# Kernel tuning notes

Hardware: AMD Instinct MI355X
Metric: run time of the kernel (lower is better)

Reference implementation:

```python
import math
import jax, jax.numpy as jnp
import numpy as np

I_DIM = 64
N_MODES = 16
FACTOR = 4
EPS = 1e-5


def group_norm(x, w, b):
    # x: [B, M, N, C] channels-last; torch GroupNorm(C//16, C) over (group_channels, M, N)
    B, M, N, C = x.shape
    g = C // 16
    xr = x.reshape(B, M, N, g, C // g)
    mean = xr.mean(axis=(1, 2, 4), keepdims=True)
    var = xr.var(axis=(1, 2, 4), keepdims=True)
    xr = (xr - mean) * jax.lax.rsqrt(var + EPS)
    return xr.reshape(B, M, N, C) * w + b


def feed_forward(x, res, l1w, l1b, l2w, l2b, g1w, g1b, g2w, g2b, g3w, g3b):
    h = x @ l1w + l1b                      # [B,M,N,C*factor]
    h = group_norm(h, g1w, g1b)            # fork_1
    h = jax.nn.relu(h)
    h = h @ l2w + l2b                      # [B,M,N,C]
    h = group_norm(h, g2w, g2b)            # fork_2
    h = res + h
    h = group_norm(h, g3w, g3b)            # fork_3
    return h


def setup_inputs() -> dict:
    key = jax.random.key(0)
    ks = jax.random.split(key, 20)
    B, M, N, I = 4, 128, 128, I_DIM
    H = I * FACTOR
    z = jax.random.normal(ks[0], (B, 2 * M * N * I, 1), dtype=jnp.float32)
    x = jax.random.normal(ks[1], (B, M * N * I, 1), dtype=jnp.float32)
    # fourier weights [in, out, nm, nm, 2], xavier-ish scale
    fw_scale = math.sqrt(2.0 / (I + I))
    fw1 = jax.random.normal(ks[2], (I, I, N_MODES, N_MODES, 2), dtype=jnp.float32) * fw_scale
    fw2 = jax.random.normal(ks[3], (I, I, N_MODES, N_MODES, 2), dtype=jnp.float32) * fw_scale
    def ff_params(k0):
        kk = jax.random.split(k0, 4)
        return dict(
            l1w=jax.random.normal(kk[0], (I, H), dtype=jnp.float32) * math.sqrt(2.0 / (I + H)),
            l1b=jnp.zeros((H,), jnp.float32),
            l2w=jax.random.normal(kk[1], (H, I), dtype=jnp.float32) * math.sqrt(2.0 / (I + H)),
            l2b=jnp.zeros((I,), jnp.float32),
            g1w=jnp.ones((H,), jnp.float32), g1b=jnp.zeros((H,), jnp.float32),
            g2w=jnp.ones((I,), jnp.float32), g2b=jnp.zeros((I,), jnp.float32),
            g3w=jnp.ones((I,), jnp.float32), g3b=jnp.zeros((I,), jnp.float32),
        )
    bp = ff_params(ks[4])
    fp = ff_params(ks[5])
    out = {"z": z, "x": x, "fw1": fw1, "fw2": fw2}
    for name, p in (("b", bp), ("f", fp)):
        for k, v in p.items():
            out[f"{name}_{k}"] = v
    return out


def reference(z, x, fw1, fw2,
              b_l1w, b_l1b, b_l2w, b_l2b, b_g1w, b_g1b, b_g2w, b_g2b, b_g3w, b_g3b,
              f_l1w, f_l1b, f_l2w, f_l2b, f_g1w, f_g1b, f_g2w, f_g2b, f_g3w, f_g3b):
    I = I_DIM
    nm = N_MODES
    B = x.shape[0]
    M = N = int(math.sqrt(x.shape[1] // I))
    x4 = x.reshape(B, M, N, I)
    z5 = z.reshape(B, 2, M, N, I)
    backcast, forecast = z5[:, 0], z5[:, 1]
    x4 = x4 - backcast
    xc = jnp.transpose(x4, (0, 3, 1, 2))          # [B, I, M, N]
    x_ft = jnp.fft.rfft2(xc, s=(M, N), norm='ortho')  # [B, I, M, N//2+1] complex64
    w1 = fw1[..., 0] + 1j * fw1[..., 1]
    w2 = fw2[..., 0] + 1j * fw2[..., 1]
    top = jnp.einsum('bixy,ioxy->boxy', x_ft[:, :, :nm, :nm], w1)
    bot = jnp.einsum('bixy,ioxy->boxy', x_ft[:, :, -nm:, :nm], w2)
    out_ft = jnp.zeros((B, I, N, M // 2 + 1), dtype=x_ft.dtype)
    out_ft = out_ft.at[:, :, :nm, :nm].set(top).at[:, :, -nm:, :nm].set(bot)
    xo = jnp.fft.irfft2(out_ft, s=(N, M), norm='ortho')  # [B, I, M, N]
    xo = jnp.transpose(xo, (0, 2, 3, 1))                  # [B, M, N, I]
    backcast = feed_forward(xo, backcast, b_l1w, b_l1b, b_l2w, b_l2b,
                            b_g1w, b_g1b, b_g2w, b_g2b, b_g3w, b_g3b)
    forecast = feed_forward(xo, forecast, f_l1w, f_l1b, f_l2w, f_l2b,
                            f_g1w, f_g1b, f_g2w, f_g2b, f_g3w, f_g3b)
    out = jnp.stack([backcast, forecast], axis=1)         # [B, 2, M, N, I]
    return out.reshape(B, 2 * M * N * I, 1)
```

## Files before the change

kernel.cpp:

```cpp
#include <hip/hip_runtime.h>
#include <hip/hip_bf16.h>

typedef __hip_bfloat16 bf16;
typedef __attribute__((ext_vector_type(8))) short short8;
typedef __attribute__((ext_vector_type(4))) float f32x4;

#define PI2 6.283185307179586f
#define EPSV 1e-5f

__device__ __forceinline__ short f2bs(float f){
  bf16 h = __float2bfloat16(f);
  short s; __builtin_memcpy(&s, &h, 2); return s;
}
__device__ __forceinline__ float s2f(short s){
  bf16 h; __builtin_memcpy(&h, &s, 2); return __bfloat162float(h);
}
__device__ __forceinline__ float4 f4add(float4 a, float4 b){ return make_float4(a.x+b.x, a.y+b.y, a.z+b.z, a.w+b.w); }
__device__ __forceinline__ float4 f4sub(float4 a, float4 b){ return make_float4(a.x-b.x, a.y-b.y, a.z-b.z, a.w-b.w); }

__global__ __launch_bounds__(256) void k_prep_ydft(
    const float* __restrict__ x, const float* __restrict__ z,
    const float* __restrict__ fw1, const float* __restrict__ fw2,
    float2* __restrict__ FWT,
    const float* __restrict__ b_l1w, const float* __restrict__ b_l1b,
    const float* __restrict__ b_l2w, const float* __restrict__ b_l2b,
    const float* __restrict__ b_g1w, const float* __restrict__ b_g1b,
    const float* __restrict__ b_g2w, const float* __restrict__ b_g2b,
    const float* __restrict__ b_g3w, const float* __restrict__ b_g3b,
    const float* __restrict__ f_l1w, const float* __restrict__ f_l1b,
    const float* __restrict__ f_l2w, const float* __restrict__ f_l2b,
    const float* __restrict__ f_g1w, const float* __restrict__ f_g1b,
    const float* __restrict__ f_g2w, const float* __restrict__ f_g2b,
    const float* __restrict__ f_g3w, const float* __restrict__ f_g3b,
    short* __restrict__ W1g, short* __restrict__ W2g,
    float2* __restrict__ TWY, float2* __restrict__ TWX,
    float* __restrict__ PB, float* __restrict__ ST,
    float2* __restrict__ Y){
  __shared__ __align__(16) char sm[36864];
  int tid = threadIdx.x;
  int bi = blockIdx.x;
  if(bi < 512){
    float2 (*PQ)[64] = (float2(*)[64])sm;
    float2 (*RS)[64] = (float2(*)[64])(sm + 16384);
    float4 (*twl)[32] = (float4(*)[32])(sm + 32768);
    int b = bi >> 7, m = bi & 127;
    const float4* xp = (const float4*)(x + ((size_t)(b*128 + m)*128)*64);
    const float4* zp = (const float4*)(z + ((size_t)((b*2 + 0)*128 + m)*128)*64);
    int i4 = tid & 15, n0 = tid >> 4;
    #pragma unroll
    for(int it = 0; it < 2; it++){
      int np = n0 + it*16;
      float4 ea = f4sub(xp[np*16 + i4],      zp[np*16 + i4]);
      float4 eb = f4sub(xp[(np+32)*16 + i4], zp[(np+32)*16 + i4]);
      float4 ec = f4sub(xp[(np+64)*16 + i4], zp[(np+64)*16 + i4]);
      float4 ed = f4sub(xp[(np+96)*16 + i4], zp[(np+96)*16 + i4]);
      float4 sac = f4add(ea, ec), sbd = f4add(eb, ed);
      float4 P = f4add(sac, sbd), Q = f4sub(sac, sbd);
      float4 R = f4sub(ea, ec),  S = f4sub(eb, ed);
      *(float4*)&PQ[np][i4*4]     = make_float4(P.x, Q.x, P.y, Q.y);
      *(float4*)&PQ[np][i4*4 + 2] = make_float4(P.z, Q.z, P.w, Q.w);
      *(float4*)&RS[np][i4*4]     = make_float4(R.x, S.x, R.y, S.y);
      *(float4*)&RS[np][i4*4 + 2] = make_float4(R.z, S.z, R.w, S.w);
    }
    {
      int kq2 = tid >> 5, np = tid & 31;
      int ky0 = (kq2 >> 1)*4 + (kq2 & 1)*2;
      float s0, c0, s1, c1;
      sincosf(PI2*(float)((ky0*np) & 127)/128.f, &s0, &c0);
      sincosf(PI2*(float)(((ky0+1)*np) & 127)/128.f, &s1, &c1);
      twl[kq2][np] = make_float4(c0, s0, c1, s1);
    }
    __syncthreads();
    int i = tid & 63, kq = tid >> 6;
    float re[4] = {0,0,0,0}, im[4] = {0,0,0,0};
    for(int np = 0; np < 32; np++){
      float2 pq = PQ[np][i];
      float2 rs = RS[np][i];
      float4 t01 = twl[kq*2][np];
      float4 t23 = twl[kq*2 + 1][np];
      re[0] += pq.x*t01.x;               im[0] -= pq.x*t01.y;
      re[1] += rs.x*t01.z - rs.y*t01.w;  im[1] -= rs.y*t01.z + rs.x*t01.w;
      re[2] += pq.y*t23.x;               im[2] -= pq.y*t23.y;
      re[3] += rs.x*t23.z + rs.y*t23.w;  im[3] += rs.y*t23.z - rs.x*t23.w;
    }
    #pragma unroll
    for(int j = 0; j < 4; j++)
      Y[((b*128 + m)*16 + kq*4 + j)*64 + i] = make_float2(re[j], im[j]);
    return;
  }
  if(bi < 1024){
    float (*Ls)[512] = (float(*)[512])sm;
    int bb = bi - 512;
    int arr = bb >> 8, rem = bb & 255;
    int i = rem >> 2, o0 = (rem & 3) * 16;
    const float* src = (arr ? fw2 : fw1) + ((size_t)(i*64 + o0))*512;
    for(int idx = tid; idx < 8192; idx += 256)
      Ls[idx >> 9][idx & 511] = src[idx];
    __syncthreads();
    int kxw = tid >> 4, ky = tid & 15;
    float2* dst = FWT + ((size_t)((arr*16 + kxw)*16 + ky))*4096 + i*64 + o0;
    for(int ol = 0; ol < 16; ol++)
      dst[ol] = make_float2(Ls[ol][tid*2], Ls[ol][tid*2 + 1]);
    return;
  }
  int i = (bi - 1024)*256 + tid;
  if(i < 32768){
    int br = i >> 14, r = i & 16383;
    int fid = r >> 9, lane = (r >> 3) & 63, e = r & 7;
    int hb = fid & 1, t = (fid >> 1) & 3, ch = fid >> 3;
    int l15 = lane & 15, quad = lane >> 4;
    int n = ch*64 + t*16 + l15;
    int k = hb*32 + quad*8 + e;
    const float* src = br ? f_l1w : b_l1w;
    W1g[i] = f2bs(src[k*256 + n]);
    return;
  }
  i -= 32768;
  if(i < 32768){
    int br = i >> 14, r = i & 16383;
    int fid = r >> 9, lane = (r >> 3) & 63, e = r & 7;
    int hb = fid & 1, t = (fid >> 1) & 3, ch = fid >> 3;
    int l15 = lane & 15, quad = lane >> 4;
    int n = t*16 + l15;
    int k = ch*64 + hb*32 + quad*8 + e;
    const float* src = br ? f_l2w : b_l2w;
    W2g[i] = f2bs(src[k*64 + n]);
    return;
  }
  i -= 32768;
  if(i < 2048){
    int ky = i >> 7, n = i & 127;
    float ang = PI2 * (float)((ky*n) & 127) / 128.0f;
    float s, c; sincosf(ang, &s, &c);
    TWY[i] = make_float2(c, s);
    return;
  }
  i -= 2048;
  if(i < 4096){
    int kp = i >> 7, m = i & 127;
    int kx = kp < 16 ? kp : 96 + kp;
    float ang = PI2 * (float)((kx*m) & 127) / 128.0f;
    float s, c; sincosf(ang, &s, &c);
    TWX[i] = make_float2(c, s);
    return;
  }
  i -= 4096;
  if(i < 384){ ST[i] = 0.f; return; }
  i -= 384;
  if(i < 2176){
    int br = i >= 1088; int o = i - br*1088;
    float* pb = PB + br*2048;
    float v;
    if(o < 256)       v = (br ? f_l1b : b_l1b)[o];
    else if(o < 512)  v = (br ? f_g1w : b_g1w)[o-256];
    else if(o < 768)  v = (br ? f_g1b : b_g1b)[o-512];
    else if(o < 832)  v = (br ? f_l2b : b_l2b)[o-768];
    else if(o < 896)  v = (br ? f_g2w : b_g2w)[o-832];
    else if(o < 960)  v = (br ? f_g2b : b_g2b)[o-896];
    else if(o < 1024) v = (br ? f_g3w : b_g3w)[o-960];
    else              v = (br ? f_g3b : b_g3b)[o-1024];
    pb[o] = v;
  }
}

__global__ __launch_bounds__(512) void k_xdft(const float2* __restrict__ Y,
                                              const float2* __restrict__ TWX,
                                              float2* __restrict__ X2){
  __shared__ float2 twl[16][64];
  __shared__ float sc[3][128][8];
  int bi = blockIdx.x;
  int b = bi >> 6, ky = (bi >> 2) & 15, half = (bi >> 1) & 1, ih = bi & 1;
  int tid = threadIdx.x;
  for(int idx = tid; idx < 1024; idx += 512)
    twl[idx >> 6][idx & 63] = TWX[(half*16 + (idx >> 6))*128 + (idx & 63)];
  __syncthreads();
  int i = ih*32 + (tid & 31), grp = (tid >> 5) & 3, mq = tid >> 7;
  const float2* yb = Y + (size_t)b*131072 + ky*64 + i;
  float re[4] = {0,0,0,0}, im[4] = {0,0,0,0};
  for(int mi = 0; mi < 16; mi++){
    int mp = mq*16 + mi;
    float2 y1 = yb[(size_t)mp*1024];
    float2 y2 = yb[(size_t)(mp + 64)*1024];
    float2 ye = make_float2(y1.x + y2.x, y1.y + y2.y);
    float2 yo = make_float2(y1.x - y2.x, y1.y - y2.y);
    float2 t0 = twl[grp*4 + 0][mp];
    float2 t1 = twl[grp*4 + 1][mp];
    float2 t2 = twl[grp*4 + 2][mp];
    float2 t3 = twl[grp*4 + 3][mp];
    re[0] += ye.x*t0.x + ye.y*t0.y;  im[0] += ye.y*t0.x - ye.x*t0.y;
    re[1] += yo.x*t1.x + yo.y*t1.y;  im[1] += yo.y*t1.x - yo.x*t1.y;
    re[2] += ye.x*t2.x + ye.y*t2.y;  im[2] += ye.y*t2.x - ye.x*t2.y;
    re[3] += yo.x*t3.x + yo.y*t3.y;  im[3] += yo.y*t3.x - yo.x*t3.y;
  }
  if(mq){
    int sl = tid & 127;
    #pragma unroll
    for(int j = 0; j < 4; j++){ sc[mq-1][sl][j] = re[j]; sc[mq-1][sl][4 + j] = im[j]; }
  }
  __syncthreads();
  if(!mq){
    const float scn = 1.0f/128.0f;
    #pragma unroll
    for(int j = 0; j < 4; j++){
      float rr = (re[j] + sc[0][tid][j] + sc[1][tid][j] + sc[2][tid][j])*scn;
      float ii = (im[j] + sc[0][tid][4+j] + sc[1][tid][4+j] + sc[2][tid][4+j])*scn;
      int kp = half*16 + grp*4 + j;
      X2[((b*32 + kp)*16 + ky)*64 + i] = make_float2(rr, ii);
    }
  }
}

__global__ __launch_bounds__(512) void k_mix(float2* __restrict__ X2,
                                             const float2* __restrict__ FWT){
  __shared__ float2 Xs[2][4][64];
  __shared__ float sc[3][2][64][8];
  int tid = threadIdx.x;
  {
    int pl = tid >> 8, bq = (tid >> 6) & 3, ii = tid & 63;
    int p = blockIdx.x*2 + pl; int kp = p >> 4, kyy = p & 15;
    Xs[pl][bq][ii] = X2[((bq*32 + kp)*16 + kyy)*64 + ii];
  }
  __syncthreads();
  int o = tid & 63, w = tid >> 6, pl = w >> 2, iq = w & 3;
  int p = blockIdx.x*2 + pl; int kp = p >> 4, ky = p & 15;
  int arr = kp < 16 ? 0 : 1, kxw = kp < 16 ? kp : kp - 16;
  const float2* wp = FWT + ((size_t)((arr*16 + kxw)*16 + ky))*4096;
  float rr[4] = {0,0,0,0}, ii[4] = {0,0,0,0};
  for(int i = iq*16; i < iq*16 + 16; i++){
    float2 wv = wp[i*64 + o];
    #pragma unroll
    for(int b = 0; b < 4; b++){
      float xr = Xs[pl][b][i].x, xi = Xs[pl][b][i].y;
      rr[b] += xr*wv.x - xi*wv.y;
      ii[b] += xr*wv.y + xi*wv.x;
    }
  }
  if(iq){
    #pragma unroll
    for(int b = 0; b < 4; b++){ sc[iq-1][pl][o][b*2] = rr[b]; sc[iq-1][pl][o][b*2 + 1] = ii[b]; }
  }
  __syncthreads();
  if(!iq){
    #pragma unroll
    for(int b = 0; b < 4; b++){
      float r2 = rr[b] + sc[0][pl][o][b*2] + sc[1][pl][o][b*2] + sc[2][pl][o][b*2];
      float i2 = ii[b] + sc[0][pl][o][b*2+1] + sc[1][pl][o][b*2+1] + sc[2][pl][o][b*2+1];
      X2[((b*32 + kp)*16 + ky)*64 + o] = make_float2(r2, i2);
    }
  }
}

__global__ __launch_bounds__(512) void k_inv1(const float2* __restrict__ OF,
                                              const float2* __restrict__ TWX,
                                              float2* __restrict__ T){
  __shared__ float2 Fl[32][16];
  __shared__ float2 twl[32][64];
  __shared__ float sc[256][16];
  int bi = blockIdx.x;
  int b = bi >> 6, ky = (bi >> 2) & 15, oq = bi & 3;
  int tid = threadIdx.x;
  {
    int kp = tid >> 4, ol = tid & 15;
    Fl[kp][ol] = OF[((b*32 + kp)*16 + ky)*64 + oq*16 + ol];
  }
  for(int idx = tid; idx < 2048; idx += 512){
    int kp = idx >> 6, ml = idx & 63;
    twl[kp][ml] = TWX[kp*128 + ml];
  }
  __syncthreads();
  int ol = tid & 15, mg = (tid >> 4) & 15, kh = tid >> 8;
  float reE[4] = {0,0,0,0}, imE[4] = {0,0,0,0};
  float reO[4] = {0,0,0,0}, imO[4] = {0,0,0,0};
  for(int ip = 0; ip < 8; ip++){
    int kp = kh*16 + ip*2;
    float2 fe = Fl[kp][ol], fo = Fl[kp + 1][ol];
    #pragma unroll
    for(int u = 0; u < 4; u++){
      float2 te = twl[kp][mg*4 + u], to = twl[kp + 1][mg*4 + u];
      reE[u] += fe.x*te.x - fe.y*te.y;
      imE[u] += fe.x*te.y + fe.y*te.x;
      reO[u] += fo.x*to.x - fo.y*to.y;
      imO[u] += fo.x*to.y + fo.y*to.x;
    }
  }
  if(kh){
    int sl = tid & 255;
    #pragma unroll
    for(int u = 0; u < 4; u++){
      sc[sl][u] = reE[u]; sc[sl][4 + u] = imE[u];
      sc[sl][8 + u] = reO[u]; sc[sl][12 + u] = imO[u];
    }
  }
  __syncthreads();
  if(!kh){
    int o = oq*16 + ol;
    #pragma unroll
    for(int u = 0; u < 4; u++){
      float rE = reE[u] + sc[tid][u],     iE = imE[u] + sc[tid][4 + u];
      float rO = reO[u] + sc[tid][8 + u], iO = imO[u] + sc[tid][12 + u];
      int ml = mg*4 + u;
      T[((b*128 + ml)*16 + ky)*64 + o]      = make_float2(rE + rO, iE + iO);
      T[((b*128 + ml + 64)*16 + ky)*64 + o] = make_float2(rE - rO, iE - iO);
    }
  }
}

__global__ __launch_bounds__(256) void k_inv2(const float2* __restrict__ T,
                                              const float2* __restrict__ TWY,
                                              bf16* __restrict__ XO,
                                              float* __restrict__ CZ){
  __shared__ float2 twl[16][64];
  int bi = blockIdx.x;
  int b = bi >> 7, m = bi & 127;
  int tid = threadIdx.x;
  int flat = bi*256 + tid;
  if(flat < 16640) CZ[flat] = 0.f;
  for(int idx = tid; idx < 1024; idx += 256)
    twl[idx >> 6][idx & 63] = TWY[(idx >> 6)*128 + (idx & 63)];
  int o = tid & 63, ng = tid >> 6;
  const float2* tp = T + ((size_t)(b*128 + m)*16)*64 + o;
  float t0a = tp[0].x;
  float ax[15], ay[15];
  #pragma unroll
  for(int u = 0; u < 15; u++){
    float2 v = tp[(u + 1)*64];
    ax[u] = 2.f*v.x; ay[u] = 2.f*v.y;
  }
  __syncthreads();
  const float scn = 1.0f/128.0f;
  bf16* xo = XO + ((size_t)(b*128 + m)*128)*64 + o;
  for(int np = ng*16; np < ng*16 + 16; np++){
    float A = t0a, B = 0.f;
    #pragma unroll
    for(int u = 0; u < 15; u++){
      float2 t = twl[u + 1][np];
      float pr = ax[u]*t.x - ay[u]*t.y;
      if(u & 1) A += pr; else B += pr;
    }
    xo[(size_t)np*64]        = __float2bfloat16((A + B)*scn);
    xo[(size_t)(np + 64)*64] = __float2bfloat16((A - B)*scn);
  }
}

__global__ __launch_bounds__(256) void k_cov(const bf16* __restrict__ XO,
                                             float* __restrict__ Cg,
                                             float* __restrict__ SX){
  __shared__ short XT[64][264];
  __shared__ float sxl[64];
  int tid = threadIdx.x;
  int b = blockIdx.x >> 5, ck = blockIdx.x & 31;
  if(tid < 64) sxl[tid] = 0.f;
  float sxp[8];
  #pragma unroll
  for(int e = 0; e < 8; e++) sxp[e] = 0.f;
  int c0 = (tid & 7)*8;
  int lane = tid & 63, w = tid >> 6, l15 = lane & 15, quad = lane >> 4;
  f32x4 acc[4];
  #pragma unroll
  for(int tj = 0; tj < 4; tj++) acc[tj] = (f32x4){0.f,0.f,0.f,0.f};
  for(int st = 0; st < 2; st++){
    size_t pbase = (size_t)b*16384 + (size_t)ck*512 + st*256;
    const short* xg = (const short*)XO + pbase*64;
    __syncthreads();
    for(int it = 0; it < 8; it++){
      int p = it*32 + (tid >> 3);
      short8 v = *(const short8*)(xg + (size_t)p*64 + c0);
      #pragma unroll
      for(int e = 0; e < 8; e++){
        XT[c0+e][p] = v[e];
        sxp[e] += s2f(v[e]);
      }
    }
    __syncthreads();
    for(int kk = 0; kk < 8; kk++){
      short8 a = *(const short8*)&XT[w*16 + l15][kk*32 + quad*8];
      #pragma unroll
      for(int tj = 0; tj < 4; tj++){
        short8 bfr = *(const short8*)&XT[tj*16 + l15][kk*32 + quad*8];
        acc[tj] = __builtin_amdgcn_mfma_f32_16x16x32_bf16(a, bfr, acc[tj], 0, 0, 0);
      }
    }
  }
  #pragma unroll
  for(int e = 0; e < 8; e++) atomicAdd(&sxl[c0+e], sxp[e]);
  __syncthreads();
  float* Cb = Cg + b*4096;
  #pragma unroll
  for(int tj = 0; tj < 4; tj++)
    #pragma unroll
    for(int r = 0; r < 4; r++)
      atomicAdd(&Cb[(w*16 + quad*4 + r)*64 + tj*16 + l15], acc[tj][r]);
  if(tid < 64) atomicAdd(&SX[b*64 + tid], sxl[tid]);
}

__global__ __launch_bounds__(256) void k_stat(const float* __restrict__ Cg,
                                              const float* __restrict__ SX,
                                              const short* __restrict__ W1g,
                                              const float* __restrict__ PB,
                                              float* __restrict__ ST){
  __shared__ float Cl[64][65];
  __shared__ float Wl[16][64];
  __shared__ float sxl[64];
  __shared__ float g2[2];
  int tid = threadIdx.x;
  int br = blockIdx.x >> 6, b = (blockIdx.x >> 4) & 3, g = blockIdx.x & 15;
  const float* Cb = Cg + b*4096;
  for(int u = tid; u < 4096; u += 256) Cl[u >> 6][u & 63] = Cb[u];
  const short* W1 = W1g + br*16384;
  for(int u = tid; u < 1024; u += 256){
    int nl = u >> 6, k = u & 63;
    int n = g*16 + nl;
    int fid = ((n >> 6)*4 + ((n >> 4) & 3))*2 + (k >> 5);
    int lane = ((k >> 3) & 3)*16 + (n & 15);
    Wl[nl][k] = s2f(W1[fid*512 + lane*8 + (k & 7)]);
  }
  if(tid < 64) sxl[tid] = SX[b*64 + tid];
  if(tid < 2) g2[tid] = 0.f;
  __syncthreads();
  int nl = tid >> 4, ic = tid & 15;
  float qa = 0.f, sa = 0.f;
  for(int io = 0; io < 4; io++){
    int i = ic*4 + io;
    float wi = Wl[nl][i];
    float dot = 0.f;
    #pragma unroll 8
    for(int j = 0; j < 64; j++) dot += Cl[i][j]*Wl[nl][j];
    qa += wi*dot;
    sa += wi*sxl[i];
  }
  for(int off = 8; off; off >>= 1){
    qa += __shfl_xor(qa, off);
    sa += __shfl_xor(sa, off);
  }
  if(ic == 0){
    float bn = PB[br*2048 + g*16 + nl];
    float hs = sa + 16384.f*bn;
    float hq = qa + 2.f*bn*sa + 16384.f*bn*bn;
    atomicAdd(&g2[0], hs); atomicAdd(&g2[1], hq);
  }
  __syncthreads();
  if(tid == 0){
    float* S1 = ST + br*192;
    S1[(b*16 + g)*2]     = g2[0];
    S1[(b*16 + g)*2 + 1] = g2[1];
  }
}

__global__ __launch_bounds__(256, 2) void k_ffmain(const bf16* __restrict__ XO,
                                                   const short* __restrict__ W1g,
                                                   const short* __restrict__ W2g,
                                                   const float* __restrict__ PB,
                                                   const float* __restrict__ ST,
                                                   const float* __restrict__ z,
                                                   float* __restrict__ CS,
                                                   float* __restrict__ out){
  __shared__ short Ws1[16384];
  __shared__ short Ws2[16384];
  __shared__ short Hn[64][72];
  __shared__ float mu1[16], rs1[16];
  __shared__ float cs[5][64];
  int tid = threadIdx.x;
  int br = blockIdx.x >> 8, rb = blockIdx.x & 255;
  int r0 = rb << 8, b = rb >> 6;
  const float* pb = PB + br*2048;
  int lane = tid & 63, w = tid >> 6, l15 = lane & 15, quad = lane >> 4;
  int myrow = w*16 + l15;
  short8 a0r[4], a1r[4];
  #pragma unroll
  for(int c = 0; c < 4; c++){
    const short* xop = (const short*)XO + ((size_t)(r0 + c*64 + myrow))*64;
    a0r[c] = *(const short8*)(xop + quad*8);
    a1r[c] = *(const short8*)(xop + 32 + quad*8);
  }
  {
    const uint4* g1 = (const uint4*)(W1g + br*16384);
    const uint4* g2w = (const uint4*)(W2g + br*16384);
    uint4* s1 = (uint4*)Ws1; uint4* s2 = (uint4*)Ws2;
    #pragma unroll
    for(int u = 0; u < 8; u++){
      s1[u*256 + tid] = g1[u*256 + tid];
      s2[u*256 + tid] = g2w[u*256 + tid];
    }
  }
  if(tid < 16){
    const float cnt = 262144.f;
    const float* S1 = ST + br*192;
    float s = S1[(b*16 + tid)*2], q = S1[(b*16 + tid)*2 + 1];
    float mean = s/cnt, var = q/cnt - mean*mean;
    mu1[tid] = mean; rs1[tid] = rsqrtf(fmaxf(var, 0.f) + EPSV);
  }
  {
    float* c1 = &cs[0][0];
    c1[tid] = 0.f;
    if(tid < 64) c1[256 + tid] = 0.f;
  }
  __syncthreads();
  float sh[4]  = {0,0,0,0}, sh2[4] = {0,0,0,0};
  float sz[4]  = {0,0,0,0}, sz2[4] = {0,0,0,0}, shz[4] = {0,0,0,0};
  #pragma unroll
  for(int c = 0; c < 4; c++){
    size_t obase_off = ((size_t)(b*2 + br)*16384 + (r0 & 16383) + c*64)*64;
    const float* zbase = z + obase_off;
    float zr[16];
    #pragma unroll
    for(int t = 0; t < 4; t++)
      #pragma unroll
      for(int r = 0; r < 4; r++)
        zr[t*4 + r] = zbase[(size_t)(w*16 + quad*4 + r)*64 + t*16 + l15];
    f32x4 acc2[4];
    #pragma unroll
    for(int t = 0; t < 4; t++) acc2[t] = (f32x4){0.f,0.f,0.f,0.f};
    for(int ch = 0; ch < 4; ch++){
      #pragma unroll
      for(int t = 0; t < 4; t++){
        int fid = (ch*4 + t)*2;
        short8 b0 = *(const short8*)(Ws1 + fid*512 + lane*8);
        short8 b1 = *(const short8*)(Ws1 + fid*512 + 512 + lane*8);
        f32x4 acc = {0.f,0.f,0.f,0.f};
        acc = __builtin_amdgcn_mfma_f32_16x16x32_bf16(a0r[c], b0, acc, 0, 0, 0);
        acc = __builtin_amdgcn_mfma_f32_16x16x32_bf16(a1r[c], b1, acc, 0, 0, 0);
        int n = ch*64 + t*16 + l15, gi = n >> 4;
        float w1v = pb[256 + n];
        float gwv = w1v * rs1[gi];
        float gbv = (pb[n] - mu1[gi])*rs1[gi]*w1v + pb[512 + n];
        #pragma unroll
        for(int r = 0; r < 4; r++){
          float hv = acc[r]*gwv + gbv;
          hv = hv > 0.f ? hv : 0.f;
          Hn[w*16 + quad*4 + r][t*16 + l15] = f2bs(hv);
        }
      }
      short8 ha0 = *(short8*)&Hn[myrow][quad*8];
      short8 ha1 = *(short8*)&Hn[myrow][32 + quad*8];
      #pragma unroll
      for(int t = 0; t < 4; t++){
        int fid = (ch*4 + t)*2;
        short8 b0 = *(const short8*)(Ws2 + fid*512 + lane*8);
        short8 b1 = *(const short8*)(Ws2 + fid*512 + 512 + lane*8);
        acc2[t] = __builtin_amdgcn_mfma_f32_16x16x32_bf16(ha0, b0, acc2[t], 0, 0, 0);
        acc2[t] = __builtin_amdgcn_mfma_f32_16x16x32_bf16(ha1, b1, acc2[t], 0, 0, 0);
      }
    }
    float* obase = out + obase_off;
    #pragma unroll
    for(int t = 0; t < 4; t++){
      int col = t*16 + l15;
      float bias2 = pb[768 + col];
      #pragma unroll
      for(int r = 0; r < 4; r++){
        size_t off = (size_t)(w*16 + quad*4 + r)*64 + col;
        float h2 = acc2[t][r] + bias2;
        float zv = zr[t*4 + r];
        obase[off] = h2;
        sh[t] += h2; sh2[t] += h2*h2;
        sz[t] += zv; sz2[t] += zv*zv; shz[t] += h2*zv;
      }
    }
  }
  #pragma unroll
  for(int t = 0; t < 4; t++){
    float v0 = sh[t], v1 = sh2[t], v2 = sz[t], v3 = sz2[t], v4 = shz[t];
    v0 += __shfl_xor(v0, 16); v0 += __shfl_xor(v0, 32);
    v1 += __shfl_xor(v1, 16); v1 += __shfl_xor(v1, 32);
    v2 += __shfl_xor(v2, 16); v2 += __shfl_xor(v2, 32);
    v3 += __shfl_xor(v3, 16); v3 += __shfl_xor(v3, 32);
    v4 += __shfl_xor(v4, 16); v4 += __shfl_xor(v4, 32);
    if(quad == 0){
      int ch = t*16 + l15;
      atomicAdd(&cs[0][ch], v0); atomicAdd(&cs[1][ch], v1);
      atomicAdd(&cs[2][ch], v2); atomicAdd(&cs[3][ch], v3);
      atomicAdd(&cs[4][ch], v4);
    }
  }
  __syncthreads();
  float* slab = CS + (size_t)blockIdx.x*320;
  const float* c1 = &cs[0][0];
  slab[tid] = c1[tid];
  if(tid < 64) slab[256 + tid] = c1[256 + tid];
}

__global__ __launch_bounds__(256) void k_statB(const float* __restrict__ CS,
                                               const float* __restrict__ PB,
                                               float* __restrict__ CF){
  __shared__ float chs[5][64];
  __shared__ float mu2s[4], rs2s[4], tg[4], tq[4], mu3s[4], rs3s[4];
  int br = blockIdx.x >> 2, b = blockIdx.x & 3;
  int tid = threadIdx.x;
  const float* base = CS + ((size_t)(br*256 + b*64))*320;
  float* c1 = &chs[0][0];
  for(int v = tid; v < 320; v += 256){
    float s = 0.f;
    for(int k = 0; k < 64; k++) s += base[(size_t)k*320 + v];
    c1[v] = s;
  }
  __syncthreads();
  if(tid < 4){
    float s = 0.f, q = 0.f;
    for(int o = tid*16; o < tid*16 + 16; o++){ s += chs[0][o]; q += chs[1][o]; }
    float mean = s/262144.f, var = q/262144.f - mean*mean;
    mu2s[tid] = mean; rs2s[tid] = rsqrtf(fmaxf(var, 0.f) + EPSV);
    tg[tid] = 0.f; tq[tid] = 0.f;
  }
  __syncthreads();
  const float* pb = PB + br*2048;
  if(tid < 64){
    int o = tid, g = o >> 4;
    float w2v = pb[832 + o], b2v = pb[896 + o];
    float gw = w2v*rs2s[g], gb = b2v - mu2s[g]*rs2s[g]*w2v;
    float Sh = chs[0][o], Sh2 = chs[1][o], Sz = chs[2][o], Sz2 = chs[3][o], Shz = chs[4][o];
    float st = gw*Sh + Sz + 16384.f*gb;
    float sq = gw*gw*Sh2 + Sz2 + 16384.f*gb*gb + 2.f*gw*Shz + 2.f*gw*gb*Sh + 2.f*gb*Sz;
    atomicAdd(&tg[g], st); atomicAdd(&tq[g], sq);
  }
  __syncthreads();
  if(tid < 4){
    float mean = tg[tid]/262144.f, var = tq[tid]/262144.f - mean*mean;
    mu3s[tid] = mean; rs3s[tid] = rsqrtf(fmaxf(var, 0.f) + EPSV);
  }
  __syncthreads();
  if(tid < 64){
    int o = tid, g = o >> 4;
    float w2v = pb[832 + o], b2v = pb[896 + o];
    float gw = w2v*rs2s[g], gb = b2v - mu2s[g]*rs2s[g]*w2v;
    float w3v = pb[960 + o], b3v = pb[1024 + o];
    float gw3 = w3v*rs3s[g], gb3 = b3v - mu3s[g]*rs3s[g]*w3v;
    float* cf = CF + (size_t)(br*4 + b)*192;
    cf[o]       = gw*gw3;
    cf[64 + o]  = gw3;
    cf[128 + o] = gb*gw3 + gb3;
  }
}

__global__ __launch_bounds__(256) void k_final(const float* __restrict__ z,
                                               const float* __restrict__ CF,
                                               float* __restrict__ out){
  int tid = blockIdx.x*256 + threadIdx.x;
  const float4* z4 = (const float4*)z;
  const float4* cf4 = (const float4*)CF;
  float4* o4 = (float4*)out;
  #pragma unroll
  for(int r = 0; r < 8; r++){
    int i4 = r*262144 + tid;
    int s = i4 >> 18;
    int b = s >> 1, br = s & 1;
    int cbase = (br*4 + b)*48 + (i4 & 15);
    float4 a = cf4[cbase], bb = cf4[cbase + 16], g = cf4[cbase + 32];
    float4 h = o4[i4], zv = z4[i4];
    o4[i4] = make_float4(h.x*a.x + zv.x*bb.x + g.x,
                         h.y*a.y + zv.y*bb.y + g.y,
                         h.z*a.z + zv.z*bb.z + g.z,
                         h.w*a.w + zv.w*bb.w + g.w);
  }
}

extern "C" void kernel_launch(void* const* d_in, const int* in_sizes, int n_in,
                              void* d_out, int out_size, void* d_ws, size_t ws_size,
                              hipStream_t stream){
  const float* z   = (const float*)d_in[0];
  const float* x   = (const float*)d_in[1];
  const float* fw1 = (const float*)d_in[2];
  const float* fw2 = (const float*)d_in[3];
  char* ws = (char*)d_ws;
  float2* Y   = (float2*)(ws + 0);
  float2* X2  = (float2*)(ws + 4194304);
  float2* T   = Y;
  bf16*   XO  = (bf16*)(ws + 5242880);
  float*  ST  = (float*)(ws + 13631488);
  short*  W1g = (short*)(ws + 13633536);
  short*  W2g = (short*)(ws + 13699072);
  float2* TWY = (float2*)(ws + 13764608);
  float2* TWX = (float2*)(ws + 13780992);
  float*  PB  = (float*)(ws + 13813760);
  float2* FWT = (float2*)(ws + 13830144);
  float*  Cg  = (float*)(ws + 13830144);
  float*  SX  = Cg + 16384;
  float*  CS  = (float*)(ws + 14878720);
  float*  CF  = (float*)(ws + 15927296);

  const float* p[20];
  for(int i = 0; i < 20; i++) p[i] = (const float*)d_in[4 + i];

  k_prep_ydft<<<1314, 256, 0, stream>>>(x, z, fw1, fw2, FWT,
                                  p[0],p[1],p[2],p[3],p[4],p[5],p[6],p[7],p[8],p[9],
                                  p[10],p[11],p[12],p[13],p[14],p[15],p[16],p[17],p[18],p[19],
                                  W1g, W2g, TWY, TWX, PB, ST, Y);
  k_xdft<<<256, 512, 0, stream>>>(Y, TWX, X2);
  k_mix<<<256, 512, 0, stream>>>(X2, FWT);
  k_inv1<<<256, 512, 0, stream>>>(X2, TWX, T);
  k_inv2<<<512, 256, 0, stream>>>(T, TWY, XO, Cg);
  k_cov<<<128, 256, 0, stream>>>(XO, Cg, SX);
  k_stat<<<128, 256, 0, stream>>>(Cg, SX, W1g, PB, ST);
  k_ffmain<<<512, 256, 0, stream>>>(XO, W1g, W2g, PB, ST, z, CS, (float*)d_out);
  k_statB<<<8, 256, 0, stream>>>(CS, PB, CF);
  k_final<<<1024, 256, 0, stream>>>(z, CF, (float*)d_out);
}
```

Before: 247.3 us.

## Compute GroupNorm1 stats in spectral domain, store FF output as bf16, transpose Y

Removes the covariance (k_cov) and stat kernels. The first GroupNorm's sum and sum-of-squares are now computed from the truncated Fourier coefficients via Parseval, in extra blocks of the inverse-DFT kernel. The feed-forward output is staged as bf16 in a separate buffer rather than fp32 in the output, which halves that round-trip traffic at some precision cost. The Y intermediate layout is also changed so k_xdft reads along m with a small stride instead of a large one.

Result: slower. 254.9 us (+3.1%).

```diff
diff --git a/kernel.cpp b/kernel.cpp
--- a/kernel.cpp
+++ b/kernel.cpp
@@ -85,7 +85,7 @@
     }
     #pragma unroll
     for(int j = 0; j < 4; j++)
-      Y[((b*128 + m)*16 + kq*4 + j)*64 + i] = make_float2(re[j], im[j]);
+      Y[(((size_t)b*16 + kq*4 + j)*128 + m)*64 + i] = make_float2(re[j], im[j]);
     return;
   }
   if(bi < 1024){
@@ -175,12 +175,12 @@
     twl[idx >> 6][idx & 63] = TWX[(half*16 + (idx >> 6))*128 + (idx & 63)];
   __syncthreads();
   int i = ih*32 + (tid & 31), grp = (tid >> 5) & 3, mq = tid >> 7;
-  const float2* yb = Y + (size_t)b*131072 + ky*64 + i;
+  const float2* yb = Y + ((size_t)(b*16 + ky)*128)*64 + i;
   float re[4] = {0,0,0,0}, im[4] = {0,0,0,0};
   for(int mi = 0; mi < 16; mi++){
     int mp = mq*16 + mi;
-    float2 y1 = yb[(size_t)mp*1024];
-    float2 y2 = yb[(size_t)(mp + 64)*1024];
+    float2 y1 = yb[(size_t)mp*64];
+    float2 y2 = yb[(size_t)(mp + 64)*64];
     float2 ye = make_float2(y1.x + y2.x, y1.y + y2.y);
     float2 yo = make_float2(y1.x - y2.x, y1.y - y2.y);
     float2 t0 = twl[grp*4 + 0][mp];
@@ -250,71 +250,138 @@
   }
 }
 
-__global__ __launch_bounds__(512) void k_inv1(const float2* __restrict__ OF,
-                                              const float2* __restrict__ TWX,
-                                              float2* __restrict__ T){
-  __shared__ float2 Fl[32][16];
-  __shared__ float2 twl[32][64];
-  __shared__ float sc[256][16];
+__global__ __launch_bounds__(512) void k_inv1stat(const float2* __restrict__ OF,
+                                                  const float2* __restrict__ TWX,
+                                                  const short* __restrict__ W1g,
+                                                  const float* __restrict__ PB,
+                                                  float* __restrict__ ST,
+                                                  float2* __restrict__ T){
+  __shared__ __align__(16) char smu[36864];
   int bi = blockIdx.x;
-  int b = bi >> 6, ky = (bi >> 2) & 15, oq = bi & 3;
   int tid = threadIdx.x;
+  if(bi < 256){
+    float2 (*Fl)[16]  = (float2(*)[16])smu;
+    float2 (*twl)[64] = (float2(*)[64])(smu + 4096);
+    float  (*sc)[16]  = (float(*)[16])(smu + 20480);
+    int b = bi >> 6, ky = (bi >> 2) & 15, oq = bi & 3;
+    {
+      int kp = tid >> 4, ol = tid & 15;
+      Fl[kp][ol] = OF[((b*32 + kp)*16 + ky)*64 + oq*16 + ol];
+    }
+    for(int idx = tid; idx < 2048; idx += 512){
+      int kp = idx >> 6, ml = idx & 63;
+      twl[kp][ml] = TWX[kp*128 + ml];
+    }
+    __syncthreads();
+    int ol = tid & 15, mg = (tid >> 4) & 15, kh = tid >> 8;
+    float reE[4] = {0,0,0,0}, imE[4] = {0,0,0,0};
+    float reO[4] = {0,0,0,0}, imO[4] = {0,0,0,0};
+    for(int ip = 0; ip < 8; ip++){
+      int kp = kh*16 + ip*2;
+      float2 fe = Fl[kp][ol], fo = Fl[kp + 1][ol];
+      #pragma unroll
+      for(int u = 0; u < 4; u++){
+        float2 te = twl[kp][mg*4 + u], to = twl[kp + 1][mg*4 + u];
+        reE[u] += fe.x*te.x - fe.y*te.y;
+        imE[u] += fe.x*te.y + fe.y*te.x;
+        reO[u] += fo.x*to.x - fo.y*to.y;
+        imO[u] += fo.x*to.y + fo.y*to.x;
+      }
+    }
+    if(kh){
+      int sl = tid & 255;
+      #pragma unroll
+      for(int u = 0; u < 4; u++){
+        sc[sl][u] = reE[u]; sc[sl][4 + u] = imE[u];
+        sc[sl][8 + u] = reO[u]; sc[sl][12 + u] = imO[u];
+      }
+    }
+    __syncthreads();
+    if(!kh){
+      int o = oq*16 + ol;
+      #pragma unroll
+      for(int u = 0; u < 4; u++){
+        float rE = reE[u] + sc[tid][u],     iE = imE[u] + sc[tid][4 + u];
+        float rO = reO[u] + sc[tid][8 + u], iO = imO[u] + sc[tid][12 + u];
+        int ml = mg*4 + u;
+        T[((b*128 + ml)*16 + ky)*64 + o]      = make_float2(rE + rO, iE + iO);
+        T[((b*128 + ml + 64)*16 + ky)*64 + o] = make_float2(rE - rO, iE - iO);
+      }
+    }
+    return;
+  }
   {
-    int kp = tid >> 4, ol = tid & 15;
-    Fl[kp][ol] = OF[((b*32 + kp)*16 + ky)*64 + oq*16 + ol];
-  }
-  for(int idx = tid; idx < 2048; idx += 512){
-    int kp = idx >> 6, ml = idx & 63;
-    twl[kp][ml] = TWX[kp*128 + ml];
-  }
-  __syncthreads();
-  int ol = tid & 15, mg = (tid >> 4) & 15, kh = tid >> 8;
-  float reE[4] = {0,0,0,0}, imE[4] = {0,0,0,0};
-  float reO[4] = {0,0,0,0}, imO[4] = {0,0,0,0};
-  for(int ip = 0; ip < 8; ip++){
-    int kp = kh*16 + ip*2;
-    float2 fe = Fl[kp][ol], fo = Fl[kp + 1][ol];
-    #pragma unroll
-    for(int u = 0; u < 4; u++){
-      float2 te = twl[kp][mg*4 + u], to = twl[kp + 1][mg*4 + u];
-      reE[u] += fe.x*te.x - fe.y*te.y;
-      imE[u] += fe.x*te.y + fe.y*te.x;
-      reO[u] += fo.x*to.x - fo.y*to.y;
-      imO[u] += fo.x*to.y + fo.y*to.x;
-    }
-  }
-  if(kh){
-    int sl = tid & 255;
-    #pragma unroll
-    for(int u = 0; u < 4; u++){
-      sc[sl][u] = reE[u]; sc[sl][4 + u] = imE[u];
-      sc[sl][8 + u] = reO[u]; sc[sl][12 + u] = imO[u];
-    }
-  }
-  __syncthreads();
-  if(!kh){
-    int o = oq*16 + ol;
-    #pragma unroll
-    for(int u = 0; u < 4; u++){
-      float rE = reE[u] + sc[tid][u],     iE = imE[u] + sc[tid][4 + u];
-      float rO = reO[u] + sc[tid][8 + u], iO = imO[u] + sc[tid][12 + u];
-      int ml = mg*4 + u;
-      T[((b*128 + ml)*16 + ky)*64 + o]      = make_float2(rE + rO, iE + iO);
-      T[((b*128 + ml + 64)*16 + ky)*64 + o] = make_float2(rE - rO, iE - iO);
+    float2 (*Xs2)[34] = (float2(*)[34])smu;
+    float  (*Wl)[64]  = (float(*)[64])(smu + 17408);
+    float* g2 = (float*)(smu + 21504);
+    int sb = bi - 256;
+    int br = sb >> 6, b = (sb >> 4) & 3, g = sb & 15;
+    const short* W1 = W1g + br*16384;
+    for(int u = tid; u < 1024; u += 512){
+      int nl2 = u >> 6, k = u & 63;
+      int n = g*16 + nl2;
+      int fid = ((n >> 6)*4 + ((n >> 4) & 3))*2 + (k >> 5);
+      int lane2 = ((k >> 3) & 3)*16 + (n & 15);
+      Wl[nl2][k] = s2f(W1[fid*512 + lane2*8 + (k & 7)]);
+    }
+    if(tid < 2) g2[tid] = 0.f;
+    int nl = tid >> 5, kp = tid & 31;
+    int lane = tid & 63;
+    float qa = 0.f, re0 = 0.f;
+    for(int ky = 0; ky < 16; ky++){
+      __syncthreads();
+      {
+        int skp = tid >> 4, i0 = (tid & 15)*4;
+        const float2* src = OF + ((size_t)(b*32 + skp)*16 + ky)*64 + i0;
+        #pragma unroll
+        for(int j2 = 0; j2 < 4; j2++) Xs2[i0 + j2][skp] = src[j2];
+      }
+      __syncthreads();
+      float re = 0.f, im = 0.f;
+      const float* wr = Wl[nl];
+      #pragma unroll 8
+      for(int i = 0; i < 64; i++){
+        float2 v = Xs2[i][kp];
+        re += v.x*wr[i]; im += v.y*wr[i];
+      }
+      if(ky){
+        qa += 2.f*(re*re + im*im);
+      } else {
+        int pl = (lane & 32) | ((32 - kp) & 31);
+        float pre = __shfl(re, pl);
+        float pim = __shfl(im, pl);
+        if(kp == 0){ re0 = re; qa += re*re; }
+        else if(kp == 16){ qa += 0.5f*(re*re + im*im); }
+        else if(kp < 16){
+          float ar = 0.5f*(re + pre), ai = 0.5f*(im - pim);
+          qa += 2.f*(ar*ar + ai*ai);
+        }
+      }
+    }
+    for(int off = 16; off; off >>= 1) qa += __shfl_xor(qa, off);
+    if(kp == 0){
+      float sa = 128.f*re0;
+      float bn = PB[br*2048 + g*16 + nl];
+      float hs = sa + 16384.f*bn;
+      float hq = qa + 2.f*bn*sa + 16384.f*bn*bn;
+      atomicAdd(&g2[0], hs); atomicAdd(&g2[1], hq);
+    }
+    __syncthreads();
+    if(tid == 0){
+      float* S1 = ST + br*192;
+      S1[(b*16 + g)*2]     = g2[0];
+      S1[(b*16 + g)*2 + 1] = g2[1];
     }
   }
 }
 
 __global__ __launch_bounds__(256) void k_inv2(const float2* __restrict__ T,
                                               const float2* __restrict__ TWY,
-                                              bf16* __restrict__ XO,
-                                              float* __restrict__ CZ){
+                                              bf16* __restrict__ XO){
   __shared__ float2 twl[16][64];
   int bi = blockIdx.x;
   int b = bi >> 7, m = bi & 127;
   int tid = threadIdx.x;
-  int flat = bi*256 + tid;
-  if(flat < 16640) CZ[flat] = 0.f;
   for(int idx = tid; idx < 1024; idx += 256)
     twl[idx >> 6][idx & 63] = TWY[(idx >> 6)*128 + (idx & 63)];
   int o = tid & 63, ng = tid >> 6;
@@ -342,110 +409,6 @@
   }
 }
 
-__global__ __launch_bounds__(256) void k_cov(const bf16* __restrict__ XO,
-                                             float* __restrict__ Cg,
-                                             float* __restrict__ SX){
-  __shared__ short XT[64][264];
-  __shared__ float sxl[64];
-  int tid = threadIdx.x;
-  int b = blockIdx.x >> 5, ck = blockIdx.x & 31;
-  if(tid < 64) sxl[tid] = 0.f;
-  float sxp[8];
-  #pragma unroll
-  for(int e = 0; e < 8; e++) sxp[e] = 0.f;
-  int c0 = (tid & 7)*8;
-  int lane = tid & 63, w = tid >> 6, l15 = lane & 15, quad = lane >> 4;
-  f32x4 acc[4];
-  #pragma unroll
-  for(int tj = 0; tj < 4; tj++) acc[tj] = (f32x4){0.f,0.f,0.f,0.f};
-  for(int st = 0; st < 2; st++){
-    size_t pbase = (size_t)b*16384 + (size_t)ck*512 + st*256;
-    const short* xg = (const short*)XO + pbase*64;
-    __syncthreads();
-    for(int it = 0; it < 8; it++){
-      int p = it*32 + (tid >> 3);
-      short8 v = *(const short8*)(xg + (size_t)p*64 + c0);
-      #pragma unroll
-      for(int e = 0; e < 8; e++){
-        XT[c0+e][p] = v[e];
-        sxp[e] += s2f(v[e]);
-      }
-    }
-    __syncthreads();
-    for(int kk = 0; kk < 8; kk++){
-      short8 a = *(const short8*)&XT[w*16 + l15][kk*32 + quad*8];
-      #pragma unroll
-      for(int tj = 0; tj < 4; tj++){
-        short8 bfr = *(const short8*)&XT[tj*16 + l15][kk*32 + quad*8];
-        acc[tj] = __builtin_amdgcn_mfma_f32_16x16x32_bf16(a, bfr, acc[tj], 0, 0, 0);
-      }
-    }
-  }
-  #pragma unroll
-  for(int e = 0; e < 8; e++) atomicAdd(&sxl[c0+e], sxp[e]);
-  __syncthreads();
-  float* Cb = Cg + b*4096;
-  #pragma unroll
-  for(int tj = 0; tj < 4; tj++)
-    #pragma unroll
-    for(int r = 0; r < 4; r++)
-      atomicAdd(&Cb[(w*16 + quad*4 + r)*64 + tj*16 + l15], acc[tj][r]);
-  if(tid < 64) atomicAdd(&SX[b*64 + tid], sxl[tid]);
-}
-
-__global__ __launch_bounds__(256) void k_stat(const float* __restrict__ Cg,
-                                              const float* __restrict__ SX,
-                                              const short* __restrict__ W1g,
-                                              const float* __restrict__ PB,
-                                              float* __restrict__ ST){
-  __shared__ float Cl[64][65];
-  __shared__ float Wl[16][64];
-  __shared__ float sxl[64];
-  __shared__ float g2[2];
-  int tid = threadIdx.x;
-  int br = blockIdx.x >> 6, b = (blockIdx.x >> 4) & 3, g = blockIdx.x & 15;
-  const float* Cb = Cg + b*4096;
-  for(int u = tid; u < 4096; u += 256) Cl[u >> 6][u & 63] = Cb[u];
-  const short* W1 = W1g + br*16384;
-  for(int u = tid; u < 1024; u += 256){
-    int nl = u >> 6, k = u & 63;
-    int n = g*16 + nl;
-    int fid = ((n >> 6)*4 + ((n >> 4) & 3))*2 + (k >> 5);
-    int lane = ((k >> 3) & 3)*16 + (n & 15);
-    Wl[nl][k] = s2f(W1[fid*512 + lane*8 + (k & 7)]);
-  }
-  if(tid < 64) sxl[tid] = SX[b*64 + tid];
-  if(tid < 2) g2[tid] = 0.f;
-  __syncthreads();
-  int nl = tid >> 4, ic = tid & 15;
-  float qa = 0.f, sa = 0.f;
-  for(int io = 0; io < 4; io++){
-    int i = ic*4 + io;
-    float wi = Wl[nl][i];
-    float dot = 0.f;
-    #pragma unroll 8
-    for(int j = 0; j < 64; j++) dot += Cl[i][j]*Wl[nl][j];
-    qa += wi*dot;
-    sa += wi*sxl[i];
-  }
-  for(int off = 8; off; off >>= 1){
-    qa += __shfl_xor(qa, off);
-    sa += __shfl_xor(sa, off);
-  }
-  if(ic == 0){
-    float bn = PB[br*2048 + g*16 + nl];
-    float hs = sa + 16384.f*bn;
-    float hq = qa + 2.f*bn*sa + 16384.f*bn*bn;
-    atomicAdd(&g2[0], hs); atomicAdd(&g2[1], hq);
-  }
-  __syncthreads();
-  if(tid == 0){
-    float* S1 = ST + br*192;
-    S1[(b*16 + g)*2]     = g2[0];
-    S1[(b*16 + g)*2 + 1] = g2[1];
-  }
-}
-
 __global__ __launch_bounds__(256, 2) void k_ffmain(const bf16* __restrict__ XO,
                                                    const short* __restrict__ W1g,
                                                    const short* __restrict__ W2g,
@@ -453,7 +416,7 @@
                                                    const float* __restrict__ ST,
                                                    const float* __restrict__ z,
                                                    float* __restrict__ CS,
-                                                   float* __restrict__ out){
+                                                   unsigned short* __restrict__ H2){
   __shared__ short Ws1[16384];
   __shared__ short Ws2[16384];
   __shared__ short Hn[64][72];
@@ -541,7 +504,7 @@
         acc2[t] = __builtin_amdgcn_mfma_f32_16x16x32_bf16(ha1, b1, acc2[t], 0, 0, 0);
       }
     }
-    float* obase = out + obase_off;
+    unsigned short* hbase = H2 + obase_off;
     #pragma unroll
     for(int t = 0; t < 4; t++){
       int col = t*16 + l15;
@@ -551,7 +514,7 @@
         size_t off = (size_t)(w*16 + quad*4 + r)*64 + col;
         float h2 = acc2[t][r] + bias2;
         float zv = zr[t*4 + r];
-        obase[off] = h2;
+        hbase[off] = (unsigned short)f2bs(h2);
         sh[t] += h2; sh2[t] += h2*h2;
         sz[t] += zv; sz2[t] += zv*zv; shz[t] += h2*zv;
       }
@@ -633,10 +596,12 @@
 
 __global__ __launch_bounds__(256) void k_final(const float* __restrict__ z,
                                                const float* __restrict__ CF,
+                                               const unsigned short* __restrict__ H2,
                                                float* __restrict__ out){
   int tid = blockIdx.x*256 + threadIdx.x;
   const float4* z4 = (const float4*)z;
   const float4* cf4 = (const float4*)CF;
+  const ushort4* h4 = (const ushort4*)H2;
   float4* o4 = (float4*)out;
   #pragma unroll
   for(int r = 0; r < 8; r++){
@@ -645,11 +610,12 @@
     int b = s >> 1, br = s & 1;
     int cbase = (br*4 + b)*48 + (i4 & 15);
     float4 a = cf4[cbase], bb = cf4[cbase + 16], g = cf4[cbase + 32];
-    float4 h = o4[i4], zv = z4[i4];
-    o4[i4] = make_float4(h.x*a.x + zv.x*bb.x + g.x,
-                         h.y*a.y + zv.y*bb.y + g.y,
-                         h.z*a.z + zv.z*bb.z + g.z,
-                         h.w*a.w + zv.w*bb.w + g.w);
+    ushort4 hu = h4[i4];
+    float4 zv = z4[i4];
+    o4[i4] = make_float4(s2f((short)hu.x)*a.x + zv.x*bb.x + g.x,
+                         s2f((short)hu.y)*a.y + zv.y*bb.y + g.y,
+                         s2f((short)hu.z)*a.z + zv.z*bb.z + g.z,
+                         s2f((short)hu.w)*a.w + zv.w*bb.w + g.w);
   }
 }
 
@@ -672,10 +638,9 @@
   float2* TWX = (float2*)(ws + 13780992);
   float*  PB  = (float*)(ws + 13813760);
   float2* FWT = (float2*)(ws + 13830144);
-  float*  Cg  = (float*)(ws + 13830144);
-  float*  SX  = Cg + 16384;
   float*  CS  = (float*)(ws + 14878720);
   float*  CF  = (float*)(ws + 15927296);
+  unsigned short* H2 = (unsigned short*)(ws + 16777216);
 
   const float* p[20];
   for(int i = 0; i < 20; i++) p[i] = (const float*)d_in[4 + i];
@@ -686,11 +651,9 @@
                                   W1g, W2g, TWY, TWX, PB, ST, Y);
   k_xdft<<<256, 512, 0, stream>>>(Y, TWX, X2);
   k_mix<<<256, 512, 0, stream>>>(X2, FWT);
-  k_inv1<<<256, 512, 0, stream>>>(X2, TWX, T);
-  k_inv2<<<512, 256, 0, stream>>>(T, TWY, XO, Cg);
-  k_cov<<<128, 256, 0, stream>>>(XO, Cg, SX);
-  k_stat<<<128, 256, 0, stream>>>(Cg, SX, W1g, PB, ST);
-  k_ffmain<<<512, 256, 0, stream>>>(XO, W1g, W2g, PB, ST, z, CS, (float*)d_out);
+  k_inv1stat<<<384, 512, 0, stream>>>(X2, TWX, W1g, PB, ST, T);
+  k_inv2<<<512, 256, 0, stream>>>(T, TWY, XO);
+  k_ffmain<<<512, 256, 0, stream>>>(XO, W1g, W2g, PB, ST, z, CS, H2);
   k_statB<<<8, 256, 0, stream>>>(CS, PB, CF);
-  k_final<<<1024, 256, 0, stream>>>(z, CF, (float*)d_out);
-}
+  k_final<<<1024, 256, 0, stream>>>(z, CF, H2, (float*)d_out);
+}
```
